# Kernel tuning notes

Hardware: AMD Instinct MI355X
Metric: run time of the kernel (lower is better)

The kernel has to match this reference:

```python
import jax, jax.numpy as jnp
import numpy as np

N = 50000      # nodes
E = 800000     # edges (before self-loops)
IN = 128       # in_channels
C = 64         # hidden_channels (per head)
H = 2          # heads
OUT = 40       # out_channels (classes)
SLOPE = 0.2    # PyG GATConv leaky_relu negative_slope


def setup_inputs() -> dict:
    key = jax.random.key(0)
    ks = jax.random.split(key, 12)
    def glorot(k, shape, fan):
        return (jax.random.normal(k, shape, jnp.float32) / np.float32(np.sqrt(fan)))
    x = jax.random.normal(ks[0], (N, IN), jnp.float32)
    edge_index = jax.random.randint(ks[1], (2, E), 0, N, dtype=jnp.int32)
    return {
        "x": x,
        "edge_index": edge_index,
        "W0": glorot(ks[2], (IN, H * C), IN),
        "a_src0": glorot(ks[3], (H, C), C),
        "a_dst0": glorot(ks[4], (H, C), C),
        "b0": jnp.zeros((H * C,), jnp.float32),
        "W1": glorot(ks[5], (H * C, H * C), H * C),
        "a_src1": glorot(ks[6], (H, C), C),
        "a_dst1": glorot(ks[7], (H, C), C),
        "b1": jnp.zeros((H * C,), jnp.float32),
        "lin_w": glorot(ks[8], (H * C * 2, OUT), H * C * 2),
        "lin_b": jnp.zeros((OUT,), jnp.float32),
    }


def gat_conv(x, W, a_src, a_dst, b, src, dst):
    # x: [N, F_in] -> h: [N, H, C]
    h = (x @ W).reshape(-1, H, C)
    # per-node attention logits (PyG splits a into src/dst halves)
    es = jnp.einsum("nhc,hc->nh", h, a_src)  # [N, H]
    ed = jnp.einsum("nhc,hc->nh", h, a_dst)  # [N, H]
    e = jax.nn.leaky_relu(es[src] + ed[dst], SLOPE)  # [Etot, H]
    # segment softmax over incoming edges of each destination node
    m = jax.ops.segment_max(e, dst, num_segments=N)          # [N, H]
    m = jnp.where(jnp.isneginf(m), 0.0, m)
    w = jnp.exp(e - m[dst])                                  # [Etot, H]
    denom = jax.ops.segment_sum(w, dst, num_segments=N)      # [N, H]
    alpha = w / jnp.maximum(denom[dst], 1e-16)               # [Etot, H]
    # scatter-aggregate messages: [Etot, H, C] -> [N, H, C]
    out = jax.ops.segment_sum(alpha[:, :, None] * h[src], dst, num_segments=N)
    return out.reshape(-1, H * C) + b  # concat=True over heads


def reference(x, edge_index, W0, a_src0, a_dst0, b0, W1, a_src1, a_dst1, b1, lin_w, lin_b):
    # PyG GATConv adds self-loops by default
    loops = jnp.arange(N, dtype=edge_index.dtype)
    src = jnp.concatenate([edge_index[0], loops])
    dst = jnp.concatenate([edge_index[1], loops])
    h1 = jax.nn.elu(gat_conv(x, W0, a_src0, a_dst0, b0, src, dst))   # [N, H*C]
    h2 = jax.nn.elu(gat_conv(h1, W1, a_src1, a_dst1, b1, src, dst))  # [N, H*C]
    h_cat = jnp.concatenate([h1, h2], axis=1)                        # [N, 2*H*C]
    logits = h_cat @ lin_w + lin_b                                   # [N, OUT]
    return jax.nn.log_softmax(logits, axis=1)
```

## Files before the change

### kernel.cpp

```cpp
#include <hip/hip_runtime.h>
#include <math.h>

#define NN 50000
#define E0 800000
#define ET 850000
#define NBX 200
#define NBK 196
#define TILE 4096
#define NTILES 208
#define CAP 8192

typedef unsigned int uint32;
typedef unsigned short u16;
typedef __attribute__((ext_vector_type(8))) short bf16x8;
typedef __attribute__((ext_vector_type(4))) float f32x4;

__device__ __forceinline__ u16 f2bf(float f) {
  uint32 u = __float_as_uint(f);
  return (u16)((u + 0x7FFFu + ((u >> 16) & 1u)) >> 16);
}
__device__ __forceinline__ float bflo(uint32 u) { return __uint_as_float(u << 16); }
__device__ __forceinline__ float bfhi(uint32 u) { return __uint_as_float(u & 0xFFFF0000u); }

__global__ __launch_bounds__(256) void prep_kernel(
    const float* __restrict__ x, const float* __restrict__ W0, const float* __restrict__ W1,
    const float* __restrict__ lw,
    u16* __restrict__ xb, u16* __restrict__ w0t, u16* __restrict__ w1t, u16* __restrict__ lwt)
{
  int b = blockIdx.x;
  if (b < NBX) {
    const float4* x4 = (const float4*)x;
    ushort4* xb4 = (ushort4*)xb;
    const int total = NN * 128 / 4;
    for (int i = b * 256 + threadIdx.x; i < total; i += NBX * 256) {
      float4 v = x4[i];
      ushort4 u;
      u.x = f2bf(v.x); u.y = f2bf(v.y); u.z = f2bf(v.z); u.w = f2bf(v.w);
      xb4[i] = u;
    }
  } else if (b < NBX + 2) {
    const float* W = (b == NBX) ? W0 : W1;
    u16* Wt = (b == NBX) ? w0t : w1t;
    __shared__ float tile[32][129];
    const int tid = threadIdx.x;
    for (int k0 = 0; k0 < 128; k0 += 32) {
      __syncthreads();
#pragma unroll
      for (int it = 0; it < 4; ++it) {
        int q = tid + it * 256;
        int kk = q >> 5, n4 = (q & 31) * 4;
        float4 v = *(const float4*)&W[(k0 + kk) * 128 + n4];
        tile[kk][n4 + 0] = v.x; tile[kk][n4 + 1] = v.y;
        tile[kk][n4 + 2] = v.z; tile[kk][n4 + 3] = v.w;
      }
      __syncthreads();
      int n = tid >> 1, h = (tid & 1) * 16;
      __align__(16) u16 tmp[16];
#pragma unroll
      for (int j = 0; j < 16; ++j) tmp[j] = f2bf(tile[h + j][n]);
      *(uint4*)&Wt[n * 128 + k0 + h] = *(uint4*)&tmp[0];
      *(uint4*)&Wt[n * 128 + k0 + h + 8] = *(uint4*)&tmp[8];
    }
  } else {
    const int tid = threadIdx.x;
    for (int idx = tid; idx < 48 * 256; idx += 256) {
      int j = idx >> 8, k = idx & 255;
      lwt[idx] = (j < 40) ? f2bf(lw[k * 40 + j]) : (u16)0;
    }
  }
}


__global__ void zero_int_kernel(int* __restrict__ p, int n) {
  int i = blockIdx.x * blockDim.x + threadIdx.x;
  if (i < n) p[i] = 0;
}

__global__ __launch_bounds__(256) void partition_kernel(
    const int* __restrict__ ei, int* __restrict__ gcursor, uint32* __restrict__ packed)
{
  __shared__ int hist[NBK];
  __shared__ int s[256];
  __shared__ int scanb[NBK];
  __shared__ int gofs[NBK];
  __shared__ uint32 shuf[TILE];
  __shared__ unsigned char sbkt[TILE];
  const int tid = threadIdx.x;
  const int t0 = blockIdx.x * TILE;
  for (int i = tid; i < NBK; i += 256) hist[i] = 0;
  __syncthreads();
  int myb[16]; int myr[16]; uint32 mypk[16];
#pragma unroll
  for (int i = 0; i < 16; ++i) {
    int e = t0 + i * 256 + tid;
    myb[i] = -1;
    if (e < ET) {
      int src, dst;
      if (e < E0) { src = ei[e]; dst = ei[E0 + e]; }
      else        { src = e - E0; dst = src; }
      myb[i] = dst >> 8;
      mypk[i] = ((uint32)(dst & 255) << 16) | (uint32)src;
      myr[i] = atomicAdd(&hist[myb[i]], 1);
    }
  }
  __syncthreads();
  int v = (tid < NBK) ? hist[tid] : 0;
  int val = v;
  s[tid] = val;
  __syncthreads();
#pragma unroll
  for (int off = 1; off < 256; off <<= 1) {
    int t = (tid >= off) ? s[tid - off] : 0;
    __syncthreads();
    val += t;
    s[tid] = val;
    __syncthreads();
  }
  if (tid < NBK) {
    scanb[tid] = val - v;
    gofs[tid] = (v > 0) ? atomicAdd(&gcursor[tid], v) : 0;
  }
  __syncthreads();
#pragma unroll
  for (int i = 0; i < 16; ++i) {
    if (myb[i] >= 0) {
      int slot = scanb[myb[i]] + myr[i];
      shuf[slot] = mypk[i];
      sbkt[slot] = (unsigned char)myb[i];
    }
  }
  __syncthreads();
  const int tcount = (t0 + TILE <= ET) ? TILE : (ET - t0);
  for (int i = tid; i < tcount; i += 256) {
    int b = sbkt[i];
    packed[(size_t)b * CAP + gofs[b] + (i - scanb[b])] = shuf[i];
  }
}

__global__ __launch_bounds__(256) void build_kernel(
    const uint32* __restrict__ packed, const int* __restrict__ gcursor,
    int2* __restrict__ rowinfo, int* __restrict__ csr_src)
{
  __shared__ int h[256];
  __shared__ int s[256];
  __shared__ int sc[256];
  __shared__ int cur[256];
  __shared__ int ptot_s;
  __shared__ u16 simg[CAP];
  const int b = blockIdx.x;
  const int tid = threadIdx.x;
  const int cnt = gcursor[b];
  const uint32* pk = packed + (size_t)b * CAP;
  h[tid] = 0;
  cur[tid] = 0;
  __syncthreads();
  for (int i = tid; i < cnt; i += 256) atomicAdd(&h[(pk[i] >> 16) & 255], 1);
  __syncthreads();
  const int pd = (h[tid] + 7) & ~7;
  int val = pd;
  s[tid] = val;
  __syncthreads();
#pragma unroll
  for (int off = 1; off < 256; off <<= 1) {
    int t = (tid >= off) ? s[tid - off] : 0;
    __syncthreads();
    val += t;
    s[tid] = val;
    __syncthreads();
  }
  sc[tid] = val - pd;
  if (tid == 255) ptot_s = val;
  __syncthreads();
  const int ptot = ptot_s;
  for (int i = tid; i < ptot; i += 256) simg[i] = (u16)NN;
  __syncthreads();
  for (int i = tid; i < cnt; i += 256) {
    uint32 p = pk[i];
    int dl = (p >> 16) & 255;
    int r = atomicAdd(&cur[dl], 1);
    simg[sc[dl] + r] = (u16)(p & 0xFFFFu);
  }
  __syncthreads();
  int n = b * 256 + tid;
  if (n < NN) rowinfo[n] = make_int2(b * CAP + sc[tid], pd);
  for (int i = tid; i < ptot; i += 256) csr_src[b * CAP + i] = (int)simg[i];
}

__global__ __launch_bounds__(256) void gemm_att_kernel(
    const u16* __restrict__ Xb, const u16* __restrict__ Wt,
    const float* __restrict__ avs, const float* __restrict__ avd,
    u16* __restrict__ hfeat, float* __restrict__ es, float* __restrict__ ed,
    int nnodes)
{
  __shared__ u16 Xs[64 * 136];
  __shared__ float es_s[2][64];
  __shared__ float ed_s[2][64];
  const int tid = threadIdx.x;
  const int wid = tid >> 6, lane = tid & 63;
  const int quad = lane >> 4, lc = lane & 15;
  const int n0 = blockIdx.x * 64;
  if (blockIdx.x == 0 && tid < 2) es[2 * NN + tid] = -1e30f;

#pragma unroll
  for (int it = 0; it < 4; ++it) {
    int g = tid + it * 256;
    int r = g >> 4, c8 = (g & 15) * 8;
    uint4 v = make_uint4(0u, 0u, 0u, 0u);
    if (n0 + r < nnodes) v = *(const uint4*)&Xb[(size_t)(n0 + r) * 128 + c8];
    *(uint4*)&Xs[r * 136 + c8] = v;
  }
  __syncthreads();

  f32x4 acc[8];
#pragma unroll
  for (int t = 0; t < 8; ++t) acc[t] = (f32x4){0.f, 0.f, 0.f, 0.f};
  const int arow = wid * 16 + lc;
#pragma unroll
  for (int ks = 0; ks < 4; ++ks) {
    const int k0 = ks * 32 + quad * 8;
    bf16x8 a = *(const bf16x8*)&Xs[arow * 136 + k0];
#pragma unroll
    for (int t = 0; t < 8; ++t) {
      bf16x8 b = *(const bf16x8*)&Wt[(t * 16 + lc) * 128 + k0];
      acc[t] = __builtin_amdgcn_mfma_f32_16x16x32_bf16(a, b, acc[t], 0, 0, 0);
    }
  }

  float av_s[8], av_d[8];
#pragma unroll
  for (int t = 0; t < 8; ++t) { av_s[t] = avs[t * 16 + lc]; av_d[t] = avd[t * 16 + lc]; }
#pragma unroll
  for (int r = 0; r < 4; ++r) {
    float s0 = 0.f, s1 = 0.f, d0 = 0.f, d1 = 0.f;
#pragma unroll
    for (int t = 0; t < 4; ++t) { s0 += acc[t][r] * av_s[t]; d0 += acc[t][r] * av_d[t]; }
#pragma unroll
    for (int t = 4; t < 8; ++t) { s1 += acc[t][r] * av_s[t]; d1 += acc[t][r] * av_d[t]; }
#pragma unroll
    for (int m = 1; m < 16; m <<= 1) {
      s0 += __shfl_xor(s0, m); s1 += __shfl_xor(s1, m);
      d0 += __shfl_xor(d0, m); d1 += __shfl_xor(d1, m);
    }
    if (lc == 0) {
      int row = wid * 16 + quad * 4 + r;
      es_s[0][row] = s0; es_s[1][row] = s1;
      ed_s[0][row] = d0; ed_s[1][row] = d1;
    }
  }
  __syncthreads();
  u16* hout = Xs;
#pragma unroll
  for (int t = 0; t < 8; ++t)
#pragma unroll
    for (int r = 0; r < 4; ++r)
      hout[(wid * 16 + quad * 4 + r) * 136 + t * 16 + lc] = f2bf(acc[t][r]);
  __syncthreads();
#pragma unroll
  for (int it = 0; it < 4; ++it) {
    int g = tid + it * 256;
    int r = g >> 4, c8 = (g & 15) * 8;
    if (n0 + r < nnodes)
      *(uint4*)&hfeat[(size_t)(n0 + r) * 128 + c8] = *(const uint4*)&hout[r * 136 + c8];
  }
  if (tid < 64) {
    int n = n0 + tid;
    if (n < nnodes) {
      es[n * 2 + 0] = es_s[0][tid]; es[n * 2 + 1] = es_s[1][tid];
      ed[n * 2 + 0] = ed_s[0][tid]; ed[n * 2 + 1] = ed_s[1][tid];
    }
  }
}

__global__ __launch_bounds__(256) void aggregate_kernel(
    const uint4* __restrict__ hfeat4, const float* __restrict__ es, const float* __restrict__ ed,
    const int2* __restrict__ rowinfo, const int* __restrict__ csr_src,
    const float* __restrict__ bias, u16* __restrict__ out, int nnodes)
{
  int n = (blockIdx.x * blockDim.x + threadIdx.x) >> 6;
  int lane = threadIdx.x & 63;
  if (n >= nnodes) return;
  const int eg = lane >> 4;
  const int fl = lane & 15;
  const int hd = (fl >= 8) ? 1 : 0;
  const int2 ri = rowinfo[n];
  const int nch = ri.y >> 3;
  const int j0 = ri.x + eg;
  const float edn = ed[n * 2 + hd];

  float acc[8];
#pragma unroll
  for (int t = 0; t < 8; ++t) acc[t] = 0.f;
  float den = 0.f;

  int i0A = csr_src[j0], i1A = csr_src[j0 + 4];
  float e0 = es[i0A * 2 + hd] + edn; e0 = fmaxf(e0, 0.2f * e0);
  float e1 = es[i1A * 2 + hd] + edn; e1 = fmaxf(e1, 0.2f * e1);
  float w0A = __expf(e0), w1A = __expf(e1);
  for (int c = 0;;) {
    uint4 h0 = hfeat4[(size_t)i0A * 16 + fl];
    uint4 h1 = hfeat4[(size_t)i1A * 16 + fl];
    bool more = (c + 1 < nch);
    int i0B, i1B; float w0B, w1B;
    if (more) {
      int jb = j0 + (c + 1) * 8;
      i0B = csr_src[jb]; i1B = csr_src[jb + 4];
      float f0 = es[i0B * 2 + hd] + edn; f0 = fmaxf(f0, 0.2f * f0);
      float f1 = es[i1B * 2 + hd] + edn; f1 = fmaxf(f1, 0.2f * f1);
      w0B = __expf(f0); w1B = __expf(f1);
    }
    acc[0] = fmaf(w0A, bflo(h0.x), acc[0]);
    acc[1] = fmaf(w0A, bfhi(h0.x), acc[1]);
    acc[2] = fmaf(w0A, bflo(h0.y), acc[2]);
    acc[3] = fmaf(w0A, bfhi(h0.y), acc[3]);
    acc[4] = fmaf(w0A, bflo(h0.z), acc[4]);
    acc[5] = fmaf(w0A, bfhi(h0.z), acc[5]);
    acc[6] = fmaf(w0A, bflo(h0.w), acc[6]);
    acc[7] = fmaf(w0A, bfhi(h0.w), acc[7]);
    acc[0] = fmaf(w1A, bflo(h1.x), acc[0]);
    acc[1] = fmaf(w1A, bfhi(h1.x), acc[1]);
    acc[2] = fmaf(w1A, bflo(h1.y), acc[2]);
    acc[3] = fmaf(w1A, bfhi(h1.y), acc[3]);
    acc[4] = fmaf(w1A, bflo(h1.z), acc[4]);
    acc[5] = fmaf(w1A, bfhi(h1.z), acc[5]);
    acc[6] = fmaf(w1A, bflo(h1.w), acc[6]);
    acc[7] = fmaf(w1A, bfhi(h1.w), acc[7]);
    den += w0A + w1A;
    if (!more) break;
    i0A = i0B; i1A = i1B; w0A = w0B; w1A = w1B;
    ++c;
  }

#pragma unroll
  for (int t = 0; t < 8; ++t) {
    acc[t] += __shfl_xor(acc[t], 16);
    acc[t] += __shfl_xor(acc[t], 32);
  }
  den += __shfl_xor(den, 16);
  den += __shfl_xor(den, 32);

  if (eg == 0) {
    float inv = 1.f / den;
    float4 b0 = *(const float4*)&bias[fl * 8];
    float4 b1 = *(const float4*)&bias[fl * 8 + 4];
    float bv[8] = {b0.x, b0.y, b0.z, b0.w, b1.x, b1.y, b1.z, b1.w};
    u16 pk[8];
#pragma unroll
    for (int t = 0; t < 8; ++t) {
      float v = acc[t] * inv + bv[t];
      v = (v > 0.f) ? v : (__expf(v) - 1.f);
      pk[t] = f2bf(v);
    }
    uint4 o;
    o.x = (uint32)pk[0] | ((uint32)pk[1] << 16);
    o.y = (uint32)pk[2] | ((uint32)pk[3] << 16);
    o.z = (uint32)pk[4] | ((uint32)pk[5] << 16);
    o.w = (uint32)pk[6] | ((uint32)pk[7] << 16);
    ((uint4*)out)[(size_t)n * 16 + fl] = o;
  }
}

#define FS 264
__global__ __launch_bounds__(256) void final_kernel(
    const u16* __restrict__ h1b, const u16* __restrict__ h2b,
    const u16* __restrict__ lwt, const float* __restrict__ lb,
    float* __restrict__ out, int nnodes)
{
  __shared__ u16 Hs[64 * FS];
  __shared__ u16 Ls[48 * FS];
  const int tid = threadIdx.x;
  const int wid = tid >> 6, lane = tid & 63;
  const int quad = lane >> 4, lc = lane & 15;
  const int n0 = blockIdx.x * 64;

#pragma unroll
  for (int it = 0; it < 8; ++it) {
    int g = tid + it * 256;
    int r = g >> 5, c8 = (g & 31) * 8;
    uint4 v = make_uint4(0u, 0u, 0u, 0u);
    if (n0 + r < nnodes) {
      const u16* src = (c8 < 128) ? &h1b[(size_t)(n0 + r) * 128 + c8]
                                  : &h2b[(size_t)(n0 + r) * 128 + (c8 - 128)];
      v = *(const uint4*)src;
    }
    *(uint4*)&Hs[r * FS + c8] = v;
  }
#pragma unroll
  for (int it = 0; it < 6; ++it) {
    int g = tid + it * 256;
    int r = g >> 5, c8 = (g & 31) * 8;
    *(uint4*)&Ls[r * FS + c8] = *(const uint4*)&lwt[r * 256 + c8];
  }
  __syncthreads();

  f32x4 acc[3];
#pragma unroll
  for (int t = 0; t < 3; ++t) acc[t] = (f32x4){0.f, 0.f, 0.f, 0.f};
  const int arow = wid * 16 + lc;
#pragma unroll
  for (int ks = 0; ks < 8; ++ks) {
    const int k0 = ks * 32 + quad * 8;
    bf16x8 a = *(const bf16x8*)&Hs[arow * FS + k0];
#pragma unroll
    for (int t = 0; t < 3; ++t) {
      bf16x8 b = *(const bf16x8*)&Ls[(t * 16 + lc) * FS + k0];
      acc[t] = __builtin_amdgcn_mfma_f32_16x16x32_bf16(a, b, acc[t], 0, 0, 0);
    }
  }

  float bv[3];
  bool valid[3];
#pragma unroll
  for (int t = 0; t < 3; ++t) {
    int col = t * 16 + lc;
    valid[t] = (col < 40);
    bv[t] = valid[t] ? lb[col] : 0.f;
  }
#pragma unroll
  for (int r = 0; r < 4; ++r) {
    int row = wid * 16 + quad * 4 + r;
    int n = n0 + row;
    float v[3];
    float mx = -INFINITY;
#pragma unroll
    for (int t = 0; t < 3; ++t) {
      v[t] = acc[t][r] + bv[t];
      if (valid[t]) mx = fmaxf(mx, v[t]);
    }
    mx = fmaxf(mx, __shfl_xor(mx, 1));
    mx = fmaxf(mx, __shfl_xor(mx, 2));
    mx = fmaxf(mx, __shfl_xor(mx, 4));
    mx = fmaxf(mx, __shfl_xor(mx, 8));
    float s = 0.f;
#pragma unroll
    for (int t = 0; t < 3; ++t) if (valid[t]) s += __expf(v[t] - mx);
    s += __shfl_xor(s, 1);
    s += __shfl_xor(s, 2);
    s += __shfl_xor(s, 4);
    s += __shfl_xor(s, 8);
    float lg = mx + __logf(s);
    if (n < nnodes) {
#pragma unroll
      for (int t = 0; t < 3; ++t)
        if (valid[t]) out[(size_t)n * 40 + t * 16 + lc] = v[t] - lg;
    }
  }
}


extern "C" void kernel_launch(void* const* d_in, const int* in_sizes, int n_in,
                              void* d_out, int out_size, void* d_ws, size_t ws_size,
                              hipStream_t stream) {
  const float* x   = (const float*)d_in[0];
  const int*   ei  = (const int*)d_in[1];
  const float* W0  = (const float*)d_in[2];
  const float* as0 = (const float*)d_in[3];
  const float* ad0 = (const float*)d_in[4];
  const float* b0  = (const float*)d_in[5];
  const float* W1  = (const float*)d_in[6];
  const float* as1 = (const float*)d_in[7];
  const float* ad1 = (const float*)d_in[8];
  const float* b1  = (const float*)d_in[9];
  const float* lw  = (const float*)d_in[10];
  const float* lb  = (const float*)d_in[11];
  float* out = (float*)d_out;

  char* p = (char*)d_ws;
  auto carve = [&](size_t bytes) { char* r = p; p += (bytes + 255) & ~(size_t)255; return r; };
  u16* xb     = (u16*)carve((size_t)NN * 128 * 2);
  u16* w0t    = (u16*)carve(128 * 128 * 2);
  u16* w1t    = (u16*)carve(128 * 128 * 2);
  u16* lwt    = (u16*)carve(48 * 256 * 2);
  u16* hfeat  = (u16*)carve((size_t)(NN + 1) * 128 * 2);
  u16* h1b    = (u16*)carve((size_t)NN * 128 * 2);
  u16* h2b    = (u16*)carve((size_t)NN * 128 * 2);
  float* es   = (float*)carve((size_t)(NN + 1) * 2 * 4);
  float* ed   = (float*)carve((size_t)NN * 2 * 4);
  int2* rowinfo = (int2*)carve((size_t)NN * 8);
  int* csr    = (int*)carve((size_t)NBK * CAP * 4);
  uint32* packed = (uint32*)carve((size_t)NBK * CAP * 4);
  int* gcursor = (int*)carve(NBK * 4);

  prep_kernel<<<NBX + 3, 256, 0, stream>>>(x, W0, W1, lw, xb, w0t, w1t, lwt);

  zero_int_kernel<<<1, 256, 0, stream>>>(gcursor, NBK);
  partition_kernel<<<NTILES, 256, 0, stream>>>(ei, gcursor, packed);
  build_kernel<<<NBK, 256, 0, stream>>>(packed, gcursor, rowinfo, csr);

  gemm_att_kernel<<<(NN + 63) / 64, 256, 0, stream>>>(xb, w0t, as0, ad0, hfeat, es, ed, NN);
  aggregate_kernel<<<(NN * 64 + 255) / 256, 256, 0, stream>>>((const uint4*)hfeat, es, ed, rowinfo, csr, b0, h1b, NN);
  gemm_att_kernel<<<(NN + 63) / 64, 256, 0, stream>>>(h1b, w1t, as1, ad1, hfeat, es, ed, NN);
  aggregate_kernel<<<(NN * 64 + 255) / 256, 256, 0, stream>>>((const uint4*)hfeat, es, ed, rowinfo, csr, b1, h2b, NN);
  final_kernel<<<(NN + 63) / 64, 256, 0, stream>>>(h1b, h2b, lwt, lb, out, NN);
}
```

Before: 249.7 us.

## Fuse prep with partition, drop LDS staging in GEMMs, pack aggregate FMAs

Merges the bf16 conversion/prep kernel and the edge partition kernel into one launch using a shared LDS buffer, and replaces the zero kernel with a memset. The gemm_att and final kernels now read A and B operands straight from global memory instead of staging them in LDS, removing a sync and a copy but relying on cache for reuse. The aggregate inner loop uses float2 vector FMAs so the compiler can emit packed FP32 instructions. Together these aim to cut launch overhead and LDS traffic.

```diff
diff --git a/kernel.cpp b/kernel.cpp
--- a/kernel.cpp
+++ b/kernel.cpp
@@ -14,6 +14,7 @@
 typedef unsigned short u16;
 typedef __attribute__((ext_vector_type(8))) short bf16x8;
 typedef __attribute__((ext_vector_type(4))) float f32x4;
+typedef __attribute__((ext_vector_type(2))) float f32x2;
 
 __device__ __forceinline__ u16 f2bf(float f) {
   uint32 u = __float_as_uint(f);
@@ -22,118 +23,111 @@
 __device__ __forceinline__ float bflo(uint32 u) { return __uint_as_float(u << 16); }
 __device__ __forceinline__ float bfhi(uint32 u) { return __uint_as_float(u & 0xFFFF0000u); }
 
-__global__ __launch_bounds__(256) void prep_kernel(
+__global__ __launch_bounds__(256) void partition_prep_kernel(
+    const int* __restrict__ ei, int* __restrict__ gcursor, uint32* __restrict__ packed,
     const float* __restrict__ x, const float* __restrict__ W0, const float* __restrict__ W1,
     const float* __restrict__ lw,
     u16* __restrict__ xb, u16* __restrict__ w0t, u16* __restrict__ w1t, u16* __restrict__ lwt)
 {
-  int b = blockIdx.x;
-  if (b < NBX) {
-    const float4* x4 = (const float4*)x;
-    ushort4* xb4 = (ushort4*)xb;
-    const int total = NN * 128 / 4;
-    for (int i = b * 256 + threadIdx.x; i < total; i += NBX * 256) {
-      float4 v = x4[i];
-      ushort4 u;
-      u.x = f2bf(v.x); u.y = f2bf(v.y); u.z = f2bf(v.z); u.w = f2bf(v.w);
-      xb4[i] = u;
-    }
-  } else if (b < NBX + 2) {
-    const float* W = (b == NBX) ? W0 : W1;
-    u16* Wt = (b == NBX) ? w0t : w1t;
-    __shared__ float tile[32][129];
-    const int tid = threadIdx.x;
-    for (int k0 = 0; k0 < 128; k0 += 32) {
+  __shared__ __align__(16) char smem[23872];
+  const int b = blockIdx.x;
+  const int tid = threadIdx.x;
+  if (b < NTILES) {
+    int* hist = (int*)smem;
+    int* s    = (int*)(smem + 784);
+    int* scanb = (int*)(smem + 1808);
+    int* gofs  = (int*)(smem + 2592);
+    uint32* shuf = (uint32*)(smem + 3376);
+    unsigned char* sbkt = (unsigned char*)(smem + 19760);
+    const int t0 = b * TILE;
+    for (int i = tid; i < NBK; i += 256) hist[i] = 0;
+    __syncthreads();
+    int myb[16]; int myr[16]; uint32 mypk[16];
+#pragma unroll
+    for (int i = 0; i < 16; ++i) {
+      int e = t0 + i * 256 + tid;
+      myb[i] = -1;
+      if (e < ET) {
+        int src, dst;
+        if (e < E0) { src = ei[e]; dst = ei[E0 + e]; }
+        else        { src = e - E0; dst = src; }
+        myb[i] = dst >> 8;
+        mypk[i] = ((uint32)(dst & 255) << 16) | (uint32)src;
+        myr[i] = atomicAdd(&hist[myb[i]], 1);
+      }
+    }
+    __syncthreads();
+    int v = (tid < NBK) ? hist[tid] : 0;
+    int val = v;
+    s[tid] = val;
+    __syncthreads();
+#pragma unroll
+    for (int off = 1; off < 256; off <<= 1) {
+      int t = (tid >= off) ? s[tid - off] : 0;
       __syncthreads();
-#pragma unroll
-      for (int it = 0; it < 4; ++it) {
-        int q = tid + it * 256;
-        int kk = q >> 5, n4 = (q & 31) * 4;
-        float4 v = *(const float4*)&W[(k0 + kk) * 128 + n4];
-        tile[kk][n4 + 0] = v.x; tile[kk][n4 + 1] = v.y;
-        tile[kk][n4 + 2] = v.z; tile[kk][n4 + 3] = v.w;
+      val += t;
+      s[tid] = val;
+      __syncthreads();
+    }
+    if (tid < NBK) {
+      scanb[tid] = val - v;
+      gofs[tid] = (v > 0) ? atomicAdd(&gcursor[tid], v) : 0;
+    }
+    __syncthreads();
+#pragma unroll
+    for (int i = 0; i < 16; ++i) {
+      if (myb[i] >= 0) {
+        int slot = scanb[myb[i]] + myr[i];
+        shuf[slot] = mypk[i];
+        sbkt[slot] = (unsigned char)myb[i];
       }
-      __syncthreads();
-      int n = tid >> 1, h = (tid & 1) * 16;
-      __align__(16) u16 tmp[16];
-#pragma unroll
-      for (int j = 0; j < 16; ++j) tmp[j] = f2bf(tile[h + j][n]);
-      *(uint4*)&Wt[n * 128 + k0 + h] = *(uint4*)&tmp[0];
-      *(uint4*)&Wt[n * 128 + k0 + h + 8] = *(uint4*)&tmp[8];
+    }
+    __syncthreads();
+    const int tcount = (t0 + TILE <= ET) ? TILE : (ET - t0);
+    for (int i = tid; i < tcount; i += 256) {
+      int bb = sbkt[i];
+      packed[(size_t)bb * CAP + gofs[bb] + (i - scanb[bb])] = shuf[i];
     }
   } else {
-    const int tid = threadIdx.x;
-    for (int idx = tid; idx < 48 * 256; idx += 256) {
-      int j = idx >> 8, k = idx & 255;
-      lwt[idx] = (j < 40) ? f2bf(lw[k * 40 + j]) : (u16)0;
-    }
-  }
-}
-
-
-__global__ void zero_int_kernel(int* __restrict__ p, int n) {
-  int i = blockIdx.x * blockDim.x + threadIdx.x;
-  if (i < n) p[i] = 0;
-}
-
-__global__ __launch_bounds__(256) void partition_kernel(
-    const int* __restrict__ ei, int* __restrict__ gcursor, uint32* __restrict__ packed)
-{
-  __shared__ int hist[NBK];
-  __shared__ int s[256];
-  __shared__ int scanb[NBK];
-  __shared__ int gofs[NBK];
-  __shared__ uint32 shuf[TILE];
-  __shared__ unsigned char sbkt[TILE];
-  const int tid = threadIdx.x;
-  const int t0 = blockIdx.x * TILE;
-  for (int i = tid; i < NBK; i += 256) hist[i] = 0;
-  __syncthreads();
-  int myb[16]; int myr[16]; uint32 mypk[16];
-#pragma unroll
-  for (int i = 0; i < 16; ++i) {
-    int e = t0 + i * 256 + tid;
-    myb[i] = -1;
-    if (e < ET) {
-      int src, dst;
-      if (e < E0) { src = ei[e]; dst = ei[E0 + e]; }
-      else        { src = e - E0; dst = src; }
-      myb[i] = dst >> 8;
-      mypk[i] = ((uint32)(dst & 255) << 16) | (uint32)src;
-      myr[i] = atomicAdd(&hist[myb[i]], 1);
-    }
-  }
-  __syncthreads();
-  int v = (tid < NBK) ? hist[tid] : 0;
-  int val = v;
-  s[tid] = val;
-  __syncthreads();
-#pragma unroll
-  for (int off = 1; off < 256; off <<= 1) {
-    int t = (tid >= off) ? s[tid - off] : 0;
-    __syncthreads();
-    val += t;
-    s[tid] = val;
-    __syncthreads();
-  }
-  if (tid < NBK) {
-    scanb[tid] = val - v;
-    gofs[tid] = (v > 0) ? atomicAdd(&gcursor[tid], v) : 0;
-  }
-  __syncthreads();
-#pragma unroll
-  for (int i = 0; i < 16; ++i) {
-    if (myb[i] >= 0) {
-      int slot = scanb[myb[i]] + myr[i];
-      shuf[slot] = mypk[i];
-      sbkt[slot] = (unsigned char)myb[i];
-    }
-  }
-  __syncthreads();
-  const int tcount = (t0 + TILE <= ET) ? TILE : (ET - t0);
-  for (int i = tid; i < tcount; i += 256) {
-    int b = sbkt[i];
-    packed[(size_t)b * CAP + gofs[b] + (i - scanb[b])] = shuf[i];
+    const int b2 = b - NTILES;
+    if (b2 < NBX) {
+      const float4* x4 = (const float4*)x;
+      ushort4* xb4 = (ushort4*)xb;
+      const int total = NN * 128 / 4;
+      for (int i = b2 * 256 + tid; i < total; i += NBX * 256) {
+        float4 v = x4[i];
+        ushort4 u;
+        u.x = f2bf(v.x); u.y = f2bf(v.y); u.z = f2bf(v.z); u.w = f2bf(v.w);
+        xb4[i] = u;
+      }
+    } else if (b2 < NBX + 2) {
+      const float* W = (b2 == NBX) ? W0 : W1;
+      u16* Wt = (b2 == NBX) ? w0t : w1t;
+      float (*tile)[129] = (float(*)[129])smem;
+      for (int k0 = 0; k0 < 128; k0 += 32) {
+        __syncthreads();
+#pragma unroll
+        for (int it = 0; it < 4; ++it) {
+          int q = tid + it * 256;
+          int kk = q >> 5, n4 = (q & 31) * 4;
+          float4 v = *(const float4*)&W[(k0 + kk) * 128 + n4];
+          tile[kk][n4 + 0] = v.x; tile[kk][n4 + 1] = v.y;
+          tile[kk][n4 + 2] = v.z; tile[kk][n4 + 3] = v.w;
+        }
+        __syncthreads();
+        int n = tid >> 1, h = (tid & 1) * 16;
+        __align__(16) u16 tmp[16];
+#pragma unroll
+        for (int j = 0; j < 16; ++j) tmp[j] = f2bf(tile[h + j][n]);
+        *(uint4*)&Wt[n * 128 + k0 + h] = *(uint4*)&tmp[0];
+        *(uint4*)&Wt[n * 128 + k0 + h + 8] = *(uint4*)&tmp[8];
+      }
+    } else {
+      for (int idx = tid; idx < 48 * 256; idx += 256) {
+        int j = idx >> 8, k = idx & 255;
+        lwt[idx] = (j < 40) ? f2bf(lw[k * 40 + j]) : (u16)0;
+      }
+    }
   }
 }
 
@@ -192,7 +186,7 @@
     u16* __restrict__ hfeat, float* __restrict__ es, float* __restrict__ ed,
     int nnodes)
 {
-  __shared__ u16 Xs[64 * 136];
+  __shared__ u16 hout[64 * 136];
   __shared__ float es_s[2][64];
   __shared__ float ed_s[2][64];
   const int tid = threadIdx.x;
@@ -201,24 +195,16 @@
   const int n0 = blockIdx.x * 64;
   if (blockIdx.x == 0 && tid < 2) es[2 * NN + tid] = -1e30f;
 
-#pragma unroll
-  for (int it = 0; it < 4; ++it) {
-    int g = tid + it * 256;
-    int r = g >> 4, c8 = (g & 15) * 8;
-    uint4 v = make_uint4(0u, 0u, 0u, 0u);
-    if (n0 + r < nnodes) v = *(const uint4*)&Xb[(size_t)(n0 + r) * 128 + c8];
-    *(uint4*)&Xs[r * 136 + c8] = v;
-  }
-  __syncthreads();
+  const int arow = wid * 16 + lc;
+  const int rrow = min(n0 + arow, nnodes - 1);
 
   f32x4 acc[8];
 #pragma unroll
   for (int t = 0; t < 8; ++t) acc[t] = (f32x4){0.f, 0.f, 0.f, 0.f};
-  const int arow = wid * 16 + lc;
 #pragma unroll
   for (int ks = 0; ks < 4; ++ks) {
     const int k0 = ks * 32 + quad * 8;
-    bf16x8 a = *(const bf16x8*)&Xs[arow * 136 + k0];
+    bf16x8 a = *(const bf16x8*)&Xb[(size_t)rrow * 128 + k0];
 #pragma unroll
     for (int t = 0; t < 8; ++t) {
       bf16x8 b = *(const bf16x8*)&Wt[(t * 16 + lc) * 128 + k0];
@@ -247,8 +233,6 @@
       ed_s[0][row] = d0; ed_s[1][row] = d1;
     }
   }
-  __syncthreads();
-  u16* hout = Xs;
 #pragma unroll
   for (int t = 0; t < 8; ++t)
 #pragma unroll
@@ -287,9 +271,9 @@
   const int j0 = ri.x + eg;
   const float edn = ed[n * 2 + hd];
 
-  float acc[8];
-#pragma unroll
-  for (int t = 0; t < 8; ++t) acc[t] = 0.f;
+  f32x2 acc2[4];
+#pragma unroll
+  for (int t = 0; t < 4; ++t) acc2[t] = (f32x2){0.f, 0.f};
   float den = 0.f;
 
   int i0A = csr_src[j0], i1A = csr_src[j0 + 4];
@@ -308,28 +292,25 @@
       float f1 = es[i1B * 2 + hd] + edn; f1 = fmaxf(f1, 0.2f * f1);
       w0B = __expf(f0); w1B = __expf(f1);
     }
-    acc[0] = fmaf(w0A, bflo(h0.x), acc[0]);
-    acc[1] = fmaf(w0A, bfhi(h0.x), acc[1]);
-    acc[2] = fmaf(w0A, bflo(h0.y), acc[2]);
-    acc[3] = fmaf(w0A, bfhi(h0.y), acc[3]);
-    acc[4] = fmaf(w0A, bflo(h0.z), acc[4]);
-    acc[5] = fmaf(w0A, bfhi(h0.z), acc[5]);
-    acc[6] = fmaf(w0A, bflo(h0.w), acc[6]);
-    acc[7] = fmaf(w0A, bfhi(h0.w), acc[7]);
-    acc[0] = fmaf(w1A, bflo(h1.x), acc[0]);
-    acc[1] = fmaf(w1A, bfhi(h1.x), acc[1]);
-    acc[2] = fmaf(w1A, bflo(h1.y), acc[2]);
-    acc[3] = fmaf(w1A, bfhi(h1.y), acc[3]);
-    acc[4] = fmaf(w1A, bflo(h1.z), acc[4]);
-    acc[5] = fmaf(w1A, bfhi(h1.z), acc[5]);
-    acc[6] = fmaf(w1A, bflo(h1.w), acc[6]);
-    acc[7] = fmaf(w1A, bfhi(h1.w), acc[7]);
+    f32x2 w2a = (f32x2){w0A, w0A};
+    f32x2 w2b = (f32x2){w1A, w1A};
+    f32x2 p;
+    p = (f32x2){bflo(h0.x), bfhi(h0.x)}; acc2[0] = w2a * p + acc2[0];
+    p = (f32x2){bflo(h0.y), bfhi(h0.y)}; acc2[1] = w2a * p + acc2[1];
+    p = (f32x2){bflo(h0.z), bfhi(h0.z)}; acc2[2] = w2a * p + acc2[2];
+    p = (f32x2){bflo(h0.w), bfhi(h0.w)}; acc2[3] = w2a * p + acc2[3];
+    p = (f32x2){bflo(h1.x), bfhi(h1.x)}; acc2[0] = w2b * p + acc2[0];
+    p = (f32x2){bflo(h1.y), bfhi(h1.y)}; acc2[1] = w2b * p + acc2[1];
+    p = (f32x2){bflo(h1.z), bfhi(h1.z)}; acc2[2] = w2b * p + acc2[2];
+    p = (f32x2){bflo(h1.w), bfhi(h1.w)}; acc2[3] = w2b * p + acc2[3];
     den += w0A + w1A;
     if (!more) break;
     i0A = i0B; i1A = i1B; w0A = w0B; w1A = w1B;
     ++c;
   }
 
+  float acc[8] = {acc2[0].x, acc2[0].y, acc2[1].x, acc2[1].y,
+                  acc2[2].x, acc2[2].y, acc2[3].x, acc2[3].y};
 #pragma unroll
   for (int t = 0; t < 8; ++t) {
     acc[t] += __shfl_xor(acc[t], 16);
@@ -359,50 +340,30 @@
   }
 }
 
-#define FS 264
 __global__ __launch_bounds__(256) void final_kernel(
     const u16* __restrict__ h1b, const u16* __restrict__ h2b,
     const u16* __restrict__ lwt, const float* __restrict__ lb,
     float* __restrict__ out, int nnodes)
 {
-  __shared__ u16 Hs[64 * FS];
-  __shared__ u16 Ls[48 * FS];
   const int tid = threadIdx.x;
   const int wid = tid >> 6, lane = tid & 63;
   const int quad = lane >> 4, lc = lane & 15;
   const int n0 = blockIdx.x * 64;
-
-#pragma unroll
-  for (int it = 0; it < 8; ++it) {
-    int g = tid + it * 256;
-    int r = g >> 5, c8 = (g & 31) * 8;
-    uint4 v = make_uint4(0u, 0u, 0u, 0u);
-    if (n0 + r < nnodes) {
-      const u16* src = (c8 < 128) ? &h1b[(size_t)(n0 + r) * 128 + c8]
-                                  : &h2b[(size_t)(n0 + r) * 128 + (c8 - 128)];
-      v = *(const uint4*)src;
-    }
-    *(uint4*)&Hs[r * FS + c8] = v;
-  }
-#pragma unroll
-  for (int it = 0; it < 6; ++it) {
-    int g = tid + it * 256;
-    int r = g >> 5, c8 = (g & 31) * 8;
-    *(uint4*)&Ls[r * FS + c8] = *(const uint4*)&lwt[r * 256 + c8];
-  }
-  __syncthreads();
+  const int arow = wid * 16 + lc;
+  const int rrow = min(n0 + arow, nnodes - 1);
 
   f32x4 acc[3];
 #pragma unroll
   for (int t = 0; t < 3; ++t) acc[t] = (f32x4){0.f, 0.f, 0.f, 0.f};
-  const int arow = wid * 16 + lc;
 #pragma unroll
   for (int ks = 0; ks < 8; ++ks) {
-    const int k0 = ks * 32 + quad * 8;
-    bf16x8 a = *(const bf16x8*)&Hs[arow * FS + k0];
+    const u16* hsrc = (ks < 4) ? h1b : h2b;
+    const int k0 = (ks & 3) * 32 + quad * 8;
+    const int kl = ks * 32 + quad * 8;
+    bf16x8 a = *(const bf16x8*)&hsrc[(size_t)rrow * 128 + k0];
 #pragma unroll
     for (int t = 0; t < 3; ++t) {
-      bf16x8 b = *(const bf16x8*)&Ls[(t * 16 + lc) * FS + k0];
+      bf16x8 b = *(const bf16x8*)&lwt[(t * 16 + lc) * 256 + kl];
       acc[t] = __builtin_amdgcn_mfma_f32_16x16x32_bf16(a, b, acc[t], 0, 0, 0);
     }
   }
@@ -480,10 +441,10 @@
   uint32* packed = (uint32*)carve((size_t)NBK * CAP * 4);
   int* gcursor = (int*)carve(NBK * 4);
 
-  prep_kernel<<<NBX + 3, 256, 0, stream>>>(x, W0, W1, lw, xb, w0t, w1t, lwt);
-
-  zero_int_kernel<<<1, 256, 0, stream>>>(gcursor, NBK);
-  partition_kernel<<<NTILES, 256, 0, stream>>>(ei, gcursor, packed);
+  hipMemsetAsync(gcursor, 0, NBK * 4, stream);
+
+  partition_prep_kernel<<<NTILES + NBX + 3, 256, 0, stream>>>(
+      ei, gcursor, packed, x, W0, W1, lw, xb, w0t, w1t, lwt);
   build_kernel<<<NBK, 256, 0, stream>>>(packed, gcursor, rowinfo, csr);
 
   gemm_att_kernel<<<(NN + 63) / 64, 256, 0, stream>>>(xb, w0t, as0, ad0, hfeat, es, ed, NN);
```

New measurement: 251.4 us. No clear change (+0.6%).
